# Kernel optimization log

Measured on AMD Instinct MI355X. Metric: run time of the kernel, lower is better.

## Reference

```python
import jax, jax.numpy as jnp
import numpy as np

N_GRAPH = 100000
N_CAND = 10
N_TOTAL = N_GRAPH + N_CAND
F_IN = 128
N_TYPES = 10
E = 6400000


def _p(key, shape, scale=0.05):
    return scale * jax.random.normal(key, shape, dtype=jnp.float32)


def setup_inputs() -> dict:
    key = jax.random.key(0)
    ks = jax.random.split(key, 20)
    x = jax.random.normal(ks[0], (N_GRAPH, F_IN), dtype=jnp.float32)
    candidate_set = jax.random.normal(ks[1], (N_CAND, F_IN), dtype=jnp.float32)
    edge_index = jax.random.randint(ks[2], (2, E), 0, N_GRAPH, dtype=jnp.int64)
    candidate_idx = jnp.arange(N_GRAPH, N_TOTAL, dtype=jnp.int64)  # candidate nodes appended last
    return {
        "x": x, "candidate_set": candidate_set,
        "edge_index": edge_index, "candidate_idx": candidate_idx,
        "W1": _p(ks[3], (F_IN, 16)), "b1": jnp.zeros((16,), jnp.float32),
        "W2": _p(ks[4], (16, 24)), "b2": jnp.zeros((24,), jnp.float32),
        "W3": _p(ks[5], (24, 32)), "b3": jnp.zeros((32,), jnp.float32),
        "Ws1": _p(ks[6], (32, 16)), "bs1": jnp.zeros((16,), jnp.float32),
        "Ws2": _p(ks[7], (16, N_TYPES)), "bs2": jnp.zeros((N_TYPES,), jnp.float32),
        "We1": _p(ks[8], (32, 24)), "be1": jnp.zeros((24,), jnp.float32),
        "We2": _p(ks[9], (24, N_TYPES)), "be2": jnp.zeros((N_TYPES,), jnp.float32),
    }


def _gcn(h, src, dst, W, b, n):
    # GCNConv: x' = D^{-1/2}(A+I)D^{-1/2} X W + b (self-loops added)
    h = h @ W
    deg = jax.ops.segment_sum(jnp.ones(src.shape, h.dtype), dst, num_segments=n) + 1.0
    dinv = jax.lax.rsqrt(deg)
    msg = h[src] * (dinv[src] * dinv[dst])[:, None]
    out = jax.ops.segment_sum(msg, dst, num_segments=n)
    out = out + h * (dinv * dinv)[:, None]  # self-loop term
    return out + b


def relu6(x):
    return jnp.clip(x, 0.0, 6.0)


def reference(x, candidate_set, edge_index, candidate_idx,
              W1, b1, W2, b2, W3, b3,
              Ws1, bs1, Ws2, bs2, We1, be1, We2, be2):
    n = N_TOTAL
    src, dst = edge_index[0], edge_index[1]
    h = jnp.concatenate([x, candidate_set], axis=0)  # [n, F_IN]
    h = _gcn(h, src, dst, W1, b1, n)
    h = _gcn(h, src, dst, W2, b2, n)
    h = _gcn(h, src, dst, W3, b3, n)  # [n, 32]

    start_probs = jax.nn.softmax(relu6(h @ Ws1 + bs1) @ Ws2 + bs2, axis=0)  # [n, T]
    mask = jnp.ones_like(start_probs).at[candidate_idx].set(0.0)
    start_probs = start_probs * mask
    start_probs = jnp.where(start_probs == 0.0, 1e-10, start_probs)
    k1, k2 = jax.random.split(jax.random.key(42))
    start_node = jax.random.categorical(k1, jnp.log(start_probs), axis=-1)  # [n]

    combined = jnp.concatenate([h, h[start_node]], axis=0)  # [2n, 32]
    end_probs = jax.nn.softmax(relu6(combined @ We1 + be1) @ We2 + be2, axis=0)  # [2n, T]
    end_probs = end_probs.at[start_node].set(0.0)
    end_probs = jnp.where(end_probs == 0.0, 1e-10, end_probs)
    end_node = jax.random.categorical(k2, jnp.log(end_probs), axis=-1)  # [2n]
    return (start_node, end_node, start_probs, end_probs)
```

## Files before the change

kernel.cpp:

```cpp
#include <hip/hip_runtime.h>
#include <stdint.h>

constexpr int N_GRAPH = 100000;
constexpr int N_CANDS = 10;
constexpr int NT      = N_GRAPH + N_CANDS;
constexpr int F_IN    = 128;
constexpr int NTYPES  = 10;
constexpr int NE      = 6400000;

constexpr int CB_SHIFT = 9;
constexpr int CB       = 1 << CB_SHIFT;
constexpr int NBK2     = (NT + CB - 1) / CB;
constexpr int SB       = 512;
constexpr int NMAT     = NBK2 * SB;
constexpr int NSCAN_B  = NMAT / 256;
constexpr int TMPENT_CAP = NE + NMAT * 15 + 16;

#define RNG_VARIANT 0

__device__ __forceinline__ void tf2x32(uint32_t k0, uint32_t k1, uint32_t x0, uint32_t x1,
                                       uint32_t& o0, uint32_t& o1) {
  const uint32_t ks2 = k0 ^ k1 ^ 0x1BD11BDAu;
  uint32_t v0 = x0 + k0, v1 = x1 + k1;
#define TFR(r) { v0 += v1; v1 = (v1 << (r)) | (v1 >> (32 - (r))); v1 ^= v0; }
  TFR(13) TFR(15) TFR(26) TFR(6)
  v0 += k1;  v1 += ks2 + 1u;
  TFR(17) TFR(29) TFR(16) TFR(24)
  v0 += ks2; v1 += k0 + 2u;
  TFR(13) TFR(15) TFR(26) TFR(6)
  v0 += k0;  v1 += k1 + 3u;
  TFR(17) TFR(29) TFR(16) TFR(24)
  v0 += k1;  v1 += ks2 + 4u;
  TFR(13) TFR(15) TFR(26) TFR(6)
  v0 += ks2; v1 += k0 + 5u;
#undef TFR
  o0 = v0; o1 = v1;
}

__device__ __forceinline__ void derive_keys(uint32_t& a0, uint32_t& a1,
                                            uint32_t& b0, uint32_t& b1) {
#if RNG_VARIANT == 2
  uint32_t c0, c1, d0, d1;
  tf2x32(0u, 42u, 0u, 2u, c0, c1);
  tf2x32(0u, 42u, 1u, 3u, d0, d1);
  a0 = c0; a1 = d0; b0 = c1; b1 = d1;
#else
  tf2x32(0u, 42u, 0u, 0u, a0, a1);
  tf2x32(0u, 42u, 0u, 1u, b0, b1);
#endif
}

__device__ __forceinline__ uint32_t rng_bits(uint32_t k0, uint32_t k1,
                                             uint32_t idx, uint32_t total) {
#if RNG_VARIANT == 0
  uint32_t o0, o1; tf2x32(k0, k1, 0u, idx, o0, o1); return o0 ^ o1;
#elif RNG_VARIANT == 1
  uint32_t o0, o1; tf2x32(k0, k1, 0u, idx, o0, o1); return o1;
#else
  uint32_t half = total >> 1; uint32_t o0, o1;
  if (idx < half) { tf2x32(k0, k1, idx, idx + half, o0, o1); return o0; }
  tf2x32(k0, k1, idx - half, idx, o0, o1); return o1;
#endif
}

__device__ __forceinline__ double gumbel_from_bits(uint32_t bits) {
  float uf = __uint_as_float((bits >> 9) | 0x3f800000u) - 1.0f;
  uf = fmaxf(1.17549435e-38f, uf + 1.17549435e-38f);
  return -log(-log((double)uf));
}

__device__ __forceinline__ uint32_t encf(float f) {
  uint32_t u = __float_as_uint(f);
  return u ^ ((u & 0x80000000u) ? 0xFFFFFFFFu : 0x80000000u);
}
__device__ __forceinline__ float decf(uint32_t e) {
  uint32_t u = (e & 0x80000000u) ? (e ^ 0x80000000u) : ~e;
  return __uint_as_float(u);
}

__global__ __launch_bounds__(512) void k_bcount(const int* __restrict__ dst,
                                                int* __restrict__ cntmat,
                                                int* __restrict__ cnt) {
  __shared__ int h[NBK2];
  int tid = threadIdx.x, blk = blockIdx.x;
  for (int b = tid; b < NBK2; b += 512) h[b] = 0;
  __syncthreads();
  int per = (NE + SB - 1) / SB;
  int e0 = blk * per, e1 = min(e0 + per, NE);
  for (int e = e0 + tid; e < e1; e += 512) atomicAdd(&h[dst[e] >> CB_SHIFT], 1);
  __syncthreads();
  for (int b = tid; b < NBK2; b += 512) {
    int c = h[b];
    cntmat[b * SB + blk] = (c + 15) & ~15;
    if (c) atomicAdd(&cnt[b], c);
  }
}

__global__ __launch_bounds__(256) void k_s1(int* __restrict__ cmat, int* __restrict__ partial) {
  __shared__ int sm[256];
  int t = blockIdx.x * 256 + threadIdx.x;
  int v = cmat[t];
  sm[threadIdx.x] = v;
  __syncthreads();
  #pragma unroll
  for (int s = 1; s < 256; s <<= 1) {
    int a = (threadIdx.x >= s) ? sm[threadIdx.x - s] : 0;
    __syncthreads();
    sm[threadIdx.x] += a;
    __syncthreads();
  }
  cmat[t] = sm[threadIdx.x] - v;
  if (threadIdx.x == 255) partial[blockIdx.x] = sm[255];
}

__global__ __launch_bounds__(512) void k_s2(int* __restrict__ partial, int* __restrict__ cmat) {
  __shared__ int sm[512];
  int t = threadIdx.x;
  int v = (t < NSCAN_B) ? partial[t] : 0;
  sm[t] = v;
  __syncthreads();
  #pragma unroll
  for (int s = 1; s < 512; s <<= 1) {
    int a = (t >= s) ? sm[t - s] : 0;
    __syncthreads();
    sm[t] += a;
    __syncthreads();
  }
  if (t < NSCAN_B) partial[t] = sm[t] - v;
  if (t == 511) cmat[NMAT] = sm[511];
}

__global__ __launch_bounds__(256) void k_s3(int* __restrict__ cmat, const int* __restrict__ partial) {
  int t = blockIdx.x * 256 + threadIdx.x;
  cmat[t] += partial[blockIdx.x];
}

__global__ __launch_bounds__(256) void k_rowscan(const int* __restrict__ cnt,
                                                 int* __restrict__ rowbase) {
  __shared__ int sm[256];
  int t = threadIdx.x;
  int v = (t < NBK2) ? cnt[t] : 0;
  sm[t] = v;
  __syncthreads();
  #pragma unroll
  for (int s = 1; s < 256; s <<= 1) {
    int a = (t >= s) ? sm[t - s] : 0;
    __syncthreads();
    sm[t] += a;
    __syncthreads();
  }
  if (t < NBK2) rowbase[t] = sm[t] - v;
}

__global__ __launch_bounds__(512) void k_scatter2(const int* __restrict__ src,
                                                  const int* __restrict__ dst,
                                                  const int* __restrict__ cmat,
                                                  uint32_t* __restrict__ tmpent) {
  __shared__ int lcur[NBK2];
  int tid = threadIdx.x, blk = blockIdx.x;
  for (int b = tid; b < NBK2; b += 512) lcur[b] = cmat[b * SB + blk];
  __syncthreads();
  int per = (NE + SB - 1) / SB;
  int e0 = blk * per, e1 = min(e0 + per, NE);
  for (int e = e0 + tid; e < e1; e += 512) {
    int s = src[e], d = dst[e];
    int b = d >> CB_SHIFT;
    int pos = atomicAdd(&lcur[b], 1);
    tmpent[pos] = (uint32_t)s | ((uint32_t)(d & (CB - 1)) << 17);
  }
  __syncthreads();
  for (int b = tid; b < NBK2; b += 512) {
    int p = lcur[b];
    int end = cmat[b * SB + blk + 1];
    for (; p < end; ++p) tmpent[p] = 0xFFFFFFFFu;
  }
}

__global__ __launch_bounds__(512) void k_place(const uint32_t* __restrict__ tmpent,
                                               const int* __restrict__ cmat,
                                               const int* __restrict__ rowbase,
                                               int* __restrict__ rowptr,
                                               float* __restrict__ dinv,
                                               int* __restrict__ col) {
  __shared__ int sdeg[CB];
  __shared__ int sexc[CB];
  __shared__ int sscan[CB];
  int b = blockIdx.x, tid = threadIdx.x;
  sdeg[tid] = 0;
  __syncthreads();
  int r0 = cmat[b * SB], r1 = cmat[(b + 1) * SB];
  for (int e = r0 + tid; e < r1; e += 512) {
    uint32_t v = tmpent[e];
    if (v != 0xFFFFFFFFu) atomicAdd(&sdeg[v >> 17], 1);
  }
  __syncthreads();
  int d = sdeg[tid];
  sscan[tid] = d;
  __syncthreads();
  #pragma unroll
  for (int s = 1; s < CB; s <<= 1) {
    int v = (tid >= s) ? sscan[tid - s] : 0;
    __syncthreads();
    sscan[tid] += v;
    __syncthreads();
  }
  int rb = rowbase[b];
  int incl = rb + sscan[tid];
  sexc[tid] = incl - d;
  int i = b * CB + tid;
  if (i < NT) {
    rowptr[i + 1] = incl;
    dinv[i] = (float)(1.0 / sqrt((double)(d + 1)));
  }
  if (b == 0 && tid == 0) rowptr[0] = 0;
  __syncthreads();
  for (int e = r0 + tid; e < r1; e += 512) {
    uint32_t v = tmpent[e];
    if (v != 0xFFFFFFFFu) {
      int pos = atomicAdd(&sexc[v >> 17], 1);
      col[pos] = (int)(v & 0x1FFFFu);
    }
  }
}

__global__ __launch_bounds__(256) void k_mm1(const float* __restrict__ x, const float* __restrict__ cand,
                                             const float* __restrict__ W, const float* __restrict__ dinv,
                                             float* __restrict__ zs0) {
  int gid = blockIdx.x * 256 + threadIdx.x;
  if (gid >= NT * 4) return;
  int i = gid >> 2, f4 = gid & 3;
  const float* hr = (i < N_GRAPH) ? (x + (size_t)i * F_IN)
                                  : (cand + (size_t)(i - N_GRAPH) * F_IN);
  const float4* h4 = reinterpret_cast<const float4*>(hr);
  const float4* W4 = reinterpret_cast<const float4*>(W);
  double a0 = 0.0, a1 = 0.0, a2 = 0.0, a3 = 0.0;
  #pragma unroll 8
  for (int q = 0; q < 32; ++q) {
    float4 hv = h4[q];
    float4 w0 = W4[(4 * q + 0) * 4 + f4];
    float4 w1 = W4[(4 * q + 1) * 4 + f4];
    float4 w2 = W4[(4 * q + 2) * 4 + f4];
    float4 w3 = W4[(4 * q + 3) * 4 + f4];
    a0 += (double)hv.x * w0.x + (double)hv.y * w1.x + (double)hv.z * w2.x + (double)hv.w * w3.x;
    a1 += (double)hv.x * w0.y + (double)hv.y * w1.y + (double)hv.z * w2.y + (double)hv.w * w3.y;
    a2 += (double)hv.x * w0.z + (double)hv.y * w1.z + (double)hv.z * w2.z + (double)hv.w * w3.z;
    a3 += (double)hv.x * w0.w + (double)hv.y * w1.w + (double)hv.z * w2.w + (double)hv.w * w3.w;
  }
  double di = (double)dinv[i];
  float4 o;
  o.x = (float)(a0 * di); o.y = (float)(a1 * di);
  o.z = (float)(a2 * di); o.w = (float)(a3 * di);
  reinterpret_cast<float4*>(zs0)[(size_t)i * 4 + f4] = o;
}

template <bool SQ, bool WITHW, int R>
__global__ __launch_bounds__(4 * R) void k_prop(const int* __restrict__ rowptr,
                                                const int* __restrict__ col,
                                                const float* __restrict__ zin,
                                                const float* __restrict__ win,
                                                const float* __restrict__ dinv,
                                                float* __restrict__ zout,
                                                float* __restrict__ wout,
                                                float* __restrict__ wsout) {
  int i = blockIdx.x * R + threadIdx.y;
  if (i >= NT) return;
  int fx = threadIdx.x;
  const float4* z4 = reinterpret_cast<const float4*>(zin);
  int e0 = rowptr[i], e1 = rowptr[i + 1];
  double a0 = 0.0, a1 = 0.0, a2 = 0.0, a3 = 0.0, wa = 0.0;
  int e = e0;
  for (; e + 4 <= e1; e += 4) {
    int c0 = col[e], c1 = col[e + 1], c2 = col[e + 2], c3 = col[e + 3];
    float4 v0 = z4[(size_t)c0 * 4 + fx];
    float4 v1 = z4[(size_t)c1 * 4 + fx];
    float4 v2 = z4[(size_t)c2 * 4 + fx];
    float4 v3 = z4[(size_t)c3 * 4 + fx];
    if (WITHW && fx == 0)
      wa += (double)win[c0] + (double)win[c1] + (double)win[c2] + (double)win[c3];
    a0 += (double)v0.x + (double)v1.x + (double)v2.x + (double)v3.x;
    a1 += (double)v0.y + (double)v1.y + (double)v2.y + (double)v3.y;
    a2 += (double)v0.z + (double)v1.z + (double)v2.z + (double)v3.z;
    a3 += (double)v0.w + (double)v1.w + (double)v2.w + (double)v3.w;
  }
  for (; e < e1; ++e) {
    int c = col[e];
    float4 v = z4[(size_t)c * 4 + fx];
    if (WITHW && fx == 0) wa += (double)win[c];
    a0 += (double)v.x; a1 += (double)v.y; a2 += (double)v.z; a3 += (double)v.w;
  }
  float4 s = z4[(size_t)i * 4 + fx];
  a0 += (double)s.x; a1 += (double)s.y; a2 += (double)s.z; a3 += (double)s.w;
  double di = (double)dinv[i];
  double sc = SQ ? di * di : di;
  float4 o;
  o.x = (float)(sc * a0); o.y = (float)(sc * a1);
  o.z = (float)(sc * a2); o.w = (float)(sc * a3);
  reinterpret_cast<float4*>(zout)[(size_t)i * 4 + fx] = o;
  if (WITHW && fx == 0) {
    wa += (double)win[i];
    double w = di * wa;
    wout[i]  = (float)w;
    wsout[i] = (float)(di * w);
  }
}

__global__ __launch_bounds__(512) void k_small(const float* __restrict__ W2, const float* __restrict__ b2p,
                                               const float* __restrict__ W3, const float* __restrict__ b1p,
                                               double* __restrict__ M, double* __restrict__ u,
                                               double* __restrict__ v) {
  __shared__ double t[24];
  int tid = threadIdx.x;
  if (tid < 24) {
    double a = 0.0;
    for (int k = 0; k < 16; ++k) a += (double)b1p[k] * (double)W2[k * 24 + tid];
    t[tid] = a;
  }
  if (tid >= 32 && tid < 64) {
    int o = tid - 32;
    double a = 0.0;
    for (int j = 0; j < 24; ++j) a += (double)b2p[j] * (double)W3[j * 32 + o];
    v[o] = a;
  }
  __syncthreads();
  if (tid < 32) {
    double a = 0.0;
    for (int j = 0; j < 24; ++j) a += t[j] * (double)W3[j * 32 + tid];
    u[tid] = a;
  }
  {
    int k = tid >> 5, o = tid & 31;
    double a = 0.0;
    for (int j = 0; j < 24; ++j) a += (double)W2[k * 24 + j] * (double)W3[j * 32 + o];
    M[tid] = a;
  }
}

__global__ __launch_bounds__(256) void k_epi(const float* __restrict__ z3, const float* __restrict__ w1,
                                             const float* __restrict__ w2,
                                             const double* __restrict__ M, const double* __restrict__ u,
                                             const double* __restrict__ v, const float* __restrict__ b3,
                                             float* __restrict__ H) {
  int gid = blockIdx.x * 256 + threadIdx.x;
  if (gid >= NT * 32) return;
  int i = gid >> 5, o = gid & 31;
  const float* zr = z3 + (size_t)i * 16;
  double acc = (double)b3[o] + (double)w2[i] * u[o] + (double)w1[i] * v[o];
  #pragma unroll
  for (int k = 0; k < 16; ++k) acc += (double)zr[k] * M[k * 32 + o];
  H[gid] = (float)acc;
}

template <int HID>
__global__ __launch_bounds__(256) void k_head(const float* __restrict__ H, const int* __restrict__ sn,
                                              int nrows,
                                              const float* __restrict__ Wa, const float* __restrict__ ba,
                                              const float* __restrict__ Wb, const float* __restrict__ bb,
                                              float* __restrict__ logits) {
  int i = blockIdx.x * 256 + threadIdx.x;
  if (i >= nrows) return;
  int row = (i < NT) ? i : sn[i - NT];
  const float* hr = H + (size_t)row * 32;
  float h[32];
  #pragma unroll
  for (int k = 0; k < 32; ++k) h[k] = hr[k];
  double hid[HID];
  for (int j = 0; j < HID; ++j) {
    double a = (double)ba[j];
    #pragma unroll
    for (int k = 0; k < 32; ++k) a += (double)h[k] * (double)Wa[k * HID + j];
    hid[j] = fmin(fmax(a, 0.0), 6.0);
  }
  for (int t = 0; t < NTYPES; ++t) {
    double l = (double)bb[t];
    #pragma unroll
    for (int j = 0; j < HID; ++j) l += hid[j] * (double)Wb[j * NTYPES + t];
    logits[(size_t)i * NTYPES + t] = (float)l;
  }
}

__global__ __launch_bounds__(256) void k_colmax(const float* __restrict__ L, int nrows,
                                                uint32_t* __restrict__ mb) {
  __shared__ float sm[256][NTYPES];
  float m[NTYPES];
  #pragma unroll
  for (int t = 0; t < NTYPES; ++t) m[t] = -3.402823466e38f;
  for (int r = blockIdx.x * 256 + threadIdx.x; r < nrows; r += gridDim.x * 256) {
    #pragma unroll
    for (int t = 0; t < NTYPES; ++t) m[t] = fmaxf(m[t], L[(size_t)r * NTYPES + t]);
  }
  #pragma unroll
  for (int t = 0; t < NTYPES; ++t) sm[threadIdx.x][t] = m[t];
  __syncthreads();
  for (int s = 128; s > 0; s >>= 1) {
    if (threadIdx.x < s)
      for (int t = 0; t < NTYPES; ++t)
        sm[threadIdx.x][t] = fmaxf(sm[threadIdx.x][t], sm[threadIdx.x + s][t]);
    __syncthreads();
  }
  if (threadIdx.x < NTYPES) atomicMax(&mb[threadIdx.x], encf(sm[0][threadIdx.x]));
}

__global__ __launch_bounds__(256) void k_colsum(const float* __restrict__ L, int nrows,
                                                const uint32_t* __restrict__ mb,
                                                double* __restrict__ sums) {
  __shared__ double sm[256][NTYPES];
  float mx[NTYPES];
  #pragma unroll
  for (int t = 0; t < NTYPES; ++t) mx[t] = decf(mb[t]);
  double s[NTYPES];
  #pragma unroll
  for (int t = 0; t < NTYPES; ++t) s[t] = 0.0;
  for (int r = blockIdx.x * 256 + threadIdx.x; r < nrows; r += gridDim.x * 256) {
    #pragma unroll
    for (int t = 0; t < NTYPES; ++t)
      s[t] += exp((double)L[(size_t)r * NTYPES + t] - (double)mx[t]);
  }
  #pragma unroll
  for (int t = 0; t < NTYPES; ++t) sm[threadIdx.x][t] = s[t];
  __syncthreads();
  for (int st = 128; st > 0; st >>= 1) {
    if (threadIdx.x < st)
      for (int t = 0; t < NTYPES; ++t)
        sm[threadIdx.x][t] += sm[threadIdx.x + st][t];
    __syncthreads();
  }
  if (threadIdx.x < NTYPES) atomicAdd(&sums[threadIdx.x], sm[0][threadIdx.x]);
}

__global__ __launch_bounds__(256) void k_probs_start(const float* __restrict__ L,
                                                     const uint32_t* __restrict__ mb,
                                                     const double* __restrict__ sums,
                                                     float* __restrict__ P) {
  int gid = blockIdx.x * 256 + threadIdx.x;
  if (gid >= NT * NTYPES) return;
  int i = gid / NTYPES, t = gid - i * NTYPES;
  double p = exp((double)L[gid] - (double)decf(mb[t])) / sums[t];
  float pf = (float)p;
  if (i >= N_GRAPH || pf == 0.0f) pf = 1e-10f;
  P[gid] = pf;
}

__global__ __launch_bounds__(256) void k_probs_end(const float* __restrict__ L,
                                                   const uint32_t* __restrict__ mb,
                                                   const double* __restrict__ sums,
                                                   const int* __restrict__ flags,
                                                   float* __restrict__ P) {
  int gid = blockIdx.x * 256 + threadIdx.x;
  if (gid >= 2 * NT * NTYPES) return;
  int j = gid / NTYPES, t = gid - j * NTYPES;
  double p = exp((double)L[gid] - (double)decf(mb[t])) / sums[t];
  float pf = (float)p;
  if ((j < NTYPES && flags[j]) || pf == 0.0f) pf = 1e-10f;
  P[gid] = pf;
}

__global__ __launch_bounds__(256) void k_sample_start(const float* __restrict__ probs,
                                                      float* __restrict__ outSN,
                                                      int* __restrict__ sn, int* __restrict__ flags) {
  int i = blockIdx.x * 256 + threadIdx.x;
  if (i >= NT) return;
  uint32_t a0, a1, b0, b1; derive_keys(a0, a1, b0, b1);
  double best = -1e300; int bi = 0;
  #pragma unroll
  for (int t = 0; t < NTYPES; ++t) {
    uint32_t bits = rng_bits(a0, a1, (uint32_t)(i * NTYPES + t), (uint32_t)(NT * NTYPES));
    double v = log((double)probs[(size_t)i * NTYPES + t]) + gumbel_from_bits(bits);
    if (v > best) { best = v; bi = t; }
  }
  sn[i] = bi;
  outSN[i] = (float)bi;
  flags[bi] = 1;
}

__global__ __launch_bounds__(256) void k_sample_end(const float* __restrict__ probs,
                                                    float* __restrict__ outEN) {
  int j = blockIdx.x * 256 + threadIdx.x;
  if (j >= 2 * NT) return;
  uint32_t a0, a1, b0, b1; derive_keys(a0, a1, b0, b1);
  double best = -1e300; int bi = 0;
  #pragma unroll
  for (int t = 0; t < NTYPES; ++t) {
    uint32_t bits = rng_bits(b0, b1, (uint32_t)(j * NTYPES + t), (uint32_t)(2 * NT * NTYPES));
    double v = log((double)probs[(size_t)j * NTYPES + t]) + gumbel_from_bits(bits);
    if (v > best) { best = v; bi = t; }
  }
  outEN[j] = (float)bi;
}

extern "C" void kernel_launch(void* const* d_in, const int* in_sizes, int n_in,
                              void* d_out, int out_size, void* d_ws, size_t ws_size,
                              hipStream_t stream) {
  const float* x    = (const float*)d_in[0];
  const float* cand = (const float*)d_in[1];
  const int*   ei   = (const int*)d_in[2];
  const float* W1 = (const float*)d_in[4];  const float* b1 = (const float*)d_in[5];
  const float* W2 = (const float*)d_in[6];  const float* b2 = (const float*)d_in[7];
  const float* W3 = (const float*)d_in[8];  const float* b3 = (const float*)d_in[9];
  const float* Ws1 = (const float*)d_in[10]; const float* bs1 = (const float*)d_in[11];
  const float* Ws2 = (const float*)d_in[12]; const float* bs2 = (const float*)d_in[13];
  const float* We1 = (const float*)d_in[14]; const float* be1 = (const float*)d_in[15];
  const float* We2 = (const float*)d_in[16]; const float* be2 = (const float*)d_in[17];
  float* out = (float*)d_out;
  float* outSN = out;
  float* outEN = out + NT;
  float* outPS = out + 3 * NT;
  float* outPE = out + 13 * NT;

  char* ws = (char*)d_ws;
  size_t off = 0;
  auto alloc = [&](size_t bytes) -> void* {
    void* p = ws + off;
    off += (bytes + 511) & ~(size_t)511;
    return p;
  };
  float*    dinv    = (float*)alloc((size_t)NT * 4);
  int*      rowptr  = (int*)alloc((size_t)(NT + 1) * 4);
  int*      cnt     = (int*)alloc((size_t)NBK2 * 4);
  int*      rowbase = (int*)alloc((size_t)NBK2 * 4);
  int*      cmat    = (int*)alloc((size_t)(NMAT + 1) * 4);
  int*      partial = (int*)alloc(512 * 4);
  int*      col     = (int*)alloc((size_t)NE * 4);
  char*     ublk    = (char*)alloc((size_t)TMPENT_CAP * 4);
  uint32_t* tmpent  = (uint32_t*)ublk;
  float*    zsA     = (float*)ublk;
  float*    zsB     = (float*)(ublk + (size_t)NT * 16 * 4);
  float*    Ha      = (float*)(ublk + (size_t)NT * 16 * 4 * 2);
  float*    logitsS = (float*)alloc((size_t)NT * NTYPES * 4);
  float*    logitsE = (float*)alloc((size_t)2 * NT * NTYPES * 4);
  float*    w1v     = (float*)alloc((size_t)NT * 4);
  float*    ws1v    = (float*)alloc((size_t)NT * 4);
  float*    w2v     = (float*)alloc((size_t)NT * 4);
  float*    wsd     = (float*)alloc((size_t)NT * 4);
  double*   Md      = (double*)alloc(512 * 8);
  double*   ud      = (double*)alloc(32 * 8);
  double*   vd      = (double*)alloc(32 * 8);
  int*      sn      = (int*)alloc((size_t)NT * 4);
  uint32_t* maxS    = (uint32_t*)alloc(64);
  double*   sumS    = (double*)alloc(128);
  uint32_t* maxE    = (uint32_t*)alloc(64);
  double*   sumE    = (double*)alloc(128);
  int*      flags   = (int*)alloc(64);
  (void)ws_size; (void)in_sizes; (void)n_in; (void)out_size;

  const int* srcA = ei;
  const int* dstA = ei + NE;

  const int B = 256;
  auto blocks = [](long long nthreads) { return (int)((nthreads + 255) / 256); };

  hipMemsetAsync(cnt, 0, (size_t)NBK2 * 4, stream);
  k_bcount<<<SB, 512, 0, stream>>>(dstA, cmat, cnt);
  k_s1<<<NSCAN_B, 256, 0, stream>>>(cmat, partial);
  k_s2<<<1, 512, 0, stream>>>(partial, cmat);
  k_s3<<<NSCAN_B, 256, 0, stream>>>(cmat, partial);
  k_rowscan<<<1, 256, 0, stream>>>(cnt, rowbase);
  k_scatter2<<<SB, 512, 0, stream>>>(srcA, dstA, cmat, tmpent);
  k_place<<<NBK2, 512, 0, stream>>>(tmpent, cmat, rowbase, rowptr, dinv, col);

  k_small<<<1, 512, 0, stream>>>(W2, b2, W3, b1, Md, ud, vd);
  k_mm1<<<blocks((long long)NT * 4), B, 0, stream>>>(x, cand, W1, dinv, zsA);
  const int PR = 64, PBLK = (NT + PR - 1) / PR;
  k_prop<true,  true,  PR><<<PBLK, dim3(4, PR), 0, stream>>>(rowptr, col, zsA, dinv, dinv, zsB, w1v, ws1v);
  k_prop<true,  true,  PR><<<PBLK, dim3(4, PR), 0, stream>>>(rowptr, col, zsB, ws1v, dinv, zsA, w2v, wsd);
  k_prop<false, false, PR><<<PBLK, dim3(4, PR), 0, stream>>>(rowptr, col, zsA, nullptr, dinv, zsB, nullptr, nullptr);
  k_epi<<<blocks((long long)NT * 32), B, 0, stream>>>(zsB, w1v, w2v, Md, ud, vd, b3, Ha);

  k_head<16><<<blocks(NT), B, 0, stream>>>(Ha, sn, NT, Ws1, bs1, Ws2, bs2, logitsS);
  hipMemsetAsync(maxS, 0, (size_t)((char*)flags - (char*)maxS) + 512, stream);
  k_colmax<<<512, B, 0, stream>>>(logitsS, NT, maxS);
  k_colsum<<<512, B, 0, stream>>>(logitsS, NT, maxS, sumS);
  k_probs_start<<<blocks((long long)NT * NTYPES), B, 0, stream>>>(logitsS, maxS, sumS, outPS);
  k_sample_start<<<blocks(NT), B, 0, stream>>>(outPS, outSN, sn, flags);

  k_head<24><<<blocks(2 * NT), B, 0, stream>>>(Ha, sn, 2 * NT, We1, be1, We2, be2, logitsE);
  k_colmax<<<512, B, 0, stream>>>(logitsE, 2 * NT, maxE);
  k_colsum<<<512, B, 0, stream>>>(logitsE, 2 * NT, maxE, sumE);
  k_probs_end<<<blocks((long long)2 * NT * NTYPES), B, 0, stream>>>(logitsE, maxE, sumE, flags, outPE);
  k_sample_end<<<blocks(2 * NT), B, 0, stream>>>(outPE, outEN);
}
```

Measured before the change: 868.3 us.

## Split GCN propagation into two feature halves to shrink gather working set

Feature rows are split into separate low and high 8-float arrays, and each propagation layer runs twice, once per half, so the random gather working set per pass is halved for better cache hit rates. Column index loads and output stores use nontemporal hints to avoid polluting cache, and the inner loop is unrolled by 8. The trade-off is reading the CSR column array twice per layer and launching extra kernels.

```diff
diff --git a/kernel.cpp b/kernel.cpp
--- a/kernel.cpp
+++ b/kernel.cpp
@@ -17,6 +17,8 @@
 constexpr int TMPENT_CAP = NE + NMAT * 15 + 16;
 
 #define RNG_VARIANT 0
+
+typedef float f4v __attribute__((ext_vector_type(4)));
 
 __device__ __forceinline__ void tf2x32(uint32_t k0, uint32_t k1, uint32_t x0, uint32_t x1,
                                        uint32_t& o0, uint32_t& o1) {
@@ -225,7 +227,7 @@
 
 __global__ __launch_bounds__(256) void k_mm1(const float* __restrict__ x, const float* __restrict__ cand,
                                              const float* __restrict__ W, const float* __restrict__ dinv,
-                                             float* __restrict__ zs0) {
+                                             float* __restrict__ zlo, float* __restrict__ zhi) {
   int gid = blockIdx.x * 256 + threadIdx.x;
   if (gid >= NT * 4) return;
   int i = gid >> 2, f4 = gid & 3;
@@ -250,18 +252,19 @@
   float4 o;
   o.x = (float)(a0 * di); o.y = (float)(a1 * di);
   o.z = (float)(a2 * di); o.w = (float)(a3 * di);
-  reinterpret_cast<float4*>(zs0)[(size_t)i * 4 + f4] = o;
+  if (f4 < 2) reinterpret_cast<float4*>(zlo)[(size_t)i * 2 + f4] = o;
+  else        reinterpret_cast<float4*>(zhi)[(size_t)i * 2 + (f4 - 2)] = o;
 }
 
 template <bool SQ, bool WITHW, int R>
-__global__ __launch_bounds__(4 * R) void k_prop(const int* __restrict__ rowptr,
-                                                const int* __restrict__ col,
-                                                const float* __restrict__ zin,
-                                                const float* __restrict__ win,
-                                                const float* __restrict__ dinv,
-                                                float* __restrict__ zout,
-                                                float* __restrict__ wout,
-                                                float* __restrict__ wsout) {
+__global__ __launch_bounds__(2 * R) void k_proph(const int* __restrict__ rowptr,
+                                                 const int* __restrict__ col,
+                                                 const float* __restrict__ zin,
+                                                 const float* __restrict__ win,
+                                                 const float* __restrict__ dinv,
+                                                 float* __restrict__ zout,
+                                                 float* __restrict__ wout,
+                                                 float* __restrict__ wsout) {
   int i = blockIdx.x * R + threadIdx.y;
   if (i >= NT) return;
   int fx = threadIdx.x;
@@ -269,12 +272,45 @@
   int e0 = rowptr[i], e1 = rowptr[i + 1];
   double a0 = 0.0, a1 = 0.0, a2 = 0.0, a3 = 0.0, wa = 0.0;
   int e = e0;
+  for (; e + 8 <= e1; e += 8) {
+    int c0 = __builtin_nontemporal_load(col + e);
+    int c1 = __builtin_nontemporal_load(col + e + 1);
+    int c2 = __builtin_nontemporal_load(col + e + 2);
+    int c3 = __builtin_nontemporal_load(col + e + 3);
+    int c4 = __builtin_nontemporal_load(col + e + 4);
+    int c5 = __builtin_nontemporal_load(col + e + 5);
+    int c6 = __builtin_nontemporal_load(col + e + 6);
+    int c7 = __builtin_nontemporal_load(col + e + 7);
+    float4 v0 = z4[(size_t)c0 * 2 + fx];
+    float4 v1 = z4[(size_t)c1 * 2 + fx];
+    float4 v2 = z4[(size_t)c2 * 2 + fx];
+    float4 v3 = z4[(size_t)c3 * 2 + fx];
+    float4 v4 = z4[(size_t)c4 * 2 + fx];
+    float4 v5 = z4[(size_t)c5 * 2 + fx];
+    float4 v6 = z4[(size_t)c6 * 2 + fx];
+    float4 v7 = z4[(size_t)c7 * 2 + fx];
+    if (WITHW && fx == 0) {
+      wa += (double)win[c0] + (double)win[c1] + (double)win[c2] + (double)win[c3];
+      wa += (double)win[c4] + (double)win[c5] + (double)win[c6] + (double)win[c7];
+    }
+    a0 += (double)v0.x + (double)v1.x + (double)v2.x + (double)v3.x;
+    a1 += (double)v0.y + (double)v1.y + (double)v2.y + (double)v3.y;
+    a2 += (double)v0.z + (double)v1.z + (double)v2.z + (double)v3.z;
+    a3 += (double)v0.w + (double)v1.w + (double)v2.w + (double)v3.w;
+    a0 += (double)v4.x + (double)v5.x + (double)v6.x + (double)v7.x;
+    a1 += (double)v4.y + (double)v5.y + (double)v6.y + (double)v7.y;
+    a2 += (double)v4.z + (double)v5.z + (double)v6.z + (double)v7.z;
+    a3 += (double)v4.w + (double)v5.w + (double)v6.w + (double)v7.w;
+  }
   for (; e + 4 <= e1; e += 4) {
-    int c0 = col[e], c1 = col[e + 1], c2 = col[e + 2], c3 = col[e + 3];
-    float4 v0 = z4[(size_t)c0 * 4 + fx];
-    float4 v1 = z4[(size_t)c1 * 4 + fx];
-    float4 v2 = z4[(size_t)c2 * 4 + fx];
-    float4 v3 = z4[(size_t)c3 * 4 + fx];
+    int c0 = __builtin_nontemporal_load(col + e);
+    int c1 = __builtin_nontemporal_load(col + e + 1);
+    int c2 = __builtin_nontemporal_load(col + e + 2);
+    int c3 = __builtin_nontemporal_load(col + e + 3);
+    float4 v0 = z4[(size_t)c0 * 2 + fx];
+    float4 v1 = z4[(size_t)c1 * 2 + fx];
+    float4 v2 = z4[(size_t)c2 * 2 + fx];
+    float4 v3 = z4[(size_t)c3 * 2 + fx];
     if (WITHW && fx == 0)
       wa += (double)win[c0] + (double)win[c1] + (double)win[c2] + (double)win[c3];
     a0 += (double)v0.x + (double)v1.x + (double)v2.x + (double)v3.x;
@@ -283,19 +319,19 @@
     a3 += (double)v0.w + (double)v1.w + (double)v2.w + (double)v3.w;
   }
   for (; e < e1; ++e) {
-    int c = col[e];
-    float4 v = z4[(size_t)c * 4 + fx];
+    int c = __builtin_nontemporal_load(col + e);
+    float4 v = z4[(size_t)c * 2 + fx];
     if (WITHW && fx == 0) wa += (double)win[c];
     a0 += (double)v.x; a1 += (double)v.y; a2 += (double)v.z; a3 += (double)v.w;
   }
-  float4 s = z4[(size_t)i * 4 + fx];
+  float4 s = z4[(size_t)i * 2 + fx];
   a0 += (double)s.x; a1 += (double)s.y; a2 += (double)s.z; a3 += (double)s.w;
   double di = (double)dinv[i];
   double sc = SQ ? di * di : di;
-  float4 o;
+  f4v o;
   o.x = (float)(sc * a0); o.y = (float)(sc * a1);
   o.z = (float)(sc * a2); o.w = (float)(sc * a3);
-  reinterpret_cast<float4*>(zout)[(size_t)i * 4 + fx] = o;
+  __builtin_nontemporal_store(o, reinterpret_cast<f4v*>(zout) + (size_t)i * 2 + fx);
   if (WITHW && fx == 0) {
     wa += (double)win[i];
     double w = di * wa;
@@ -335,7 +371,8 @@
   }
 }
 
-__global__ __launch_bounds__(256) void k_epi(const float* __restrict__ z3, const float* __restrict__ w1,
+__global__ __launch_bounds__(256) void k_epi(const float* __restrict__ zlo, const float* __restrict__ zhi,
+                                             const float* __restrict__ w1,
                                              const float* __restrict__ w2,
                                              const double* __restrict__ M, const double* __restrict__ u,
                                              const double* __restrict__ v, const float* __restrict__ b3,
@@ -343,10 +380,13 @@
   int gid = blockIdx.x * 256 + threadIdx.x;
   if (gid >= NT * 32) return;
   int i = gid >> 5, o = gid & 31;
-  const float* zr = z3 + (size_t)i * 16;
+  const float* zrl = zlo + (size_t)i * 8;
+  const float* zrh = zhi + (size_t)i * 8;
   double acc = (double)b3[o] + (double)w2[i] * u[o] + (double)w1[i] * v[o];
   #pragma unroll
-  for (int k = 0; k < 16; ++k) acc += (double)zr[k] * M[k * 32 + o];
+  for (int k = 0; k < 8; ++k) acc += (double)zrl[k] * M[k * 32 + o];
+  #pragma unroll
+  for (int k = 0; k < 8; ++k) acc += (double)zrh[k] * M[(k + 8) * 32 + o];
   H[gid] = (float)acc;
 }
 
@@ -522,9 +562,11 @@
   int*      col     = (int*)alloc((size_t)NE * 4);
   char*     ublk    = (char*)alloc((size_t)TMPENT_CAP * 4);
   uint32_t* tmpent  = (uint32_t*)ublk;
-  float*    zsA     = (float*)ublk;
-  float*    zsB     = (float*)(ublk + (size_t)NT * 16 * 4);
-  float*    Ha      = (float*)(ublk + (size_t)NT * 16 * 4 * 2);
+  float*    zloA    = (float*)ublk;
+  float*    zhiA    = (float*)(ublk + (size_t)NT * 8 * 4);
+  float*    zloB    = (float*)(ublk + (size_t)NT * 8 * 4 * 2);
+  float*    zhiB    = (float*)(ublk + (size_t)NT * 8 * 4 * 3);
+  float*    Ha      = (float*)(ublk + (size_t)NT * 8 * 4 * 4);
   float*    logitsS = (float*)alloc((size_t)NT * NTYPES * 4);
   float*    logitsE = (float*)alloc((size_t)2 * NT * NTYPES * 4);
   float*    w1v     = (float*)alloc((size_t)NT * 4);
@@ -558,12 +600,15 @@
   k_place<<<NBK2, 512, 0, stream>>>(tmpent, cmat, rowbase, rowptr, dinv, col);
 
   k_small<<<1, 512, 0, stream>>>(W2, b2, W3, b1, Md, ud, vd);
-  k_mm1<<<blocks((long long)NT * 4), B, 0, stream>>>(x, cand, W1, dinv, zsA);
-  const int PR = 64, PBLK = (NT + PR - 1) / PR;
-  k_prop<true,  true,  PR><<<PBLK, dim3(4, PR), 0, stream>>>(rowptr, col, zsA, dinv, dinv, zsB, w1v, ws1v);
-  k_prop<true,  true,  PR><<<PBLK, dim3(4, PR), 0, stream>>>(rowptr, col, zsB, ws1v, dinv, zsA, w2v, wsd);
-  k_prop<false, false, PR><<<PBLK, dim3(4, PR), 0, stream>>>(rowptr, col, zsA, nullptr, dinv, zsB, nullptr, nullptr);
-  k_epi<<<blocks((long long)NT * 32), B, 0, stream>>>(zsB, w1v, w2v, Md, ud, vd, b3, Ha);
+  k_mm1<<<blocks((long long)NT * 4), B, 0, stream>>>(x, cand, W1, dinv, zloA, zhiA);
+  const int PR = 128, PBLK = (NT + PR - 1) / PR;
+  k_proph<true,  true,  PR><<<PBLK, dim3(2, PR), 0, stream>>>(rowptr, col, zloA, dinv, dinv, zloB, w1v, ws1v);
+  k_proph<true,  false, PR><<<PBLK, dim3(2, PR), 0, stream>>>(rowptr, col, zhiA, nullptr, dinv, zhiB, nullptr, nullptr);
+  k_proph<true,  true,  PR><<<PBLK, dim3(2, PR), 0, stream>>>(rowptr, col, zloB, ws1v, dinv, zloA, w2v, wsd);
+  k_proph<true,  false, PR><<<PBLK, dim3(2, PR), 0, stream>>>(rowptr, col, zhiB, nullptr, dinv, zhiA, nullptr, nullptr);
+  k_proph<false, false, PR><<<PBLK, dim3(2, PR), 0, stream>>>(rowptr, col, zloA, nullptr, dinv, zloB, nullptr, nullptr);
+  k_proph<false, false, PR><<<PBLK, dim3(2, PR), 0, stream>>>(rowptr, col, zhiA, nullptr, dinv, zhiB, nullptr, nullptr);
+  k_epi<<<blocks((long long)NT * 32), B, 0, stream>>>(zloB, zhiB, w1v, w2v, Md, ud, vd, b3, Ha);
 
   k_head<16><<<blocks(NT), B, 0, stream>>>(Ha, sn, NT, Ws1, bs1, Ws2, bs2, logitsS);
   hipMemsetAsync(maxS, 0, (size_t)((char*)flags - (char*)maxS) + 512, stream);
```

New measurement: 965.1 us. 1.11x slower.

## Split each node's edges across two thread groups and fuse probability with sampling

Applied to the files above, without the earlier changes.

The propagation kernel now gives each node 8 threads instead of 4. Two 4-thread groups take alternating 4-edge chunks, and their partial sums are combined with a lane shuffle, which roughly doubles memory-level parallelism per row in the gather-bound SpMM. Column indices are loaded nontemporally to keep them out of cache. The separate softmax-probability and Gumbel-sampling kernels are merged for both the start and end heads, which saves a launch and a reread of the probability array each time. Each row now carries more serial work per thread, and the masking logic is duplicated inside the fused kernels.

```diff
diff --git a/kernel.cpp b/kernel.cpp
--- a/kernel.cpp
+++ b/kernel.cpp
@@ -17,6 +17,8 @@
 constexpr int TMPENT_CAP = NE + NMAT * 15 + 16;
 
 #define RNG_VARIANT 0
+
+typedef float f4v __attribute__((ext_vector_type(4)));
 
 __device__ __forceinline__ void tf2x32(uint32_t k0, uint32_t k1, uint32_t x0, uint32_t x1,
                                        uint32_t& o0, uint32_t& o1) {
@@ -254,53 +256,68 @@
 }
 
 template <bool SQ, bool WITHW, int R>
-__global__ __launch_bounds__(4 * R) void k_prop(const int* __restrict__ rowptr,
-                                                const int* __restrict__ col,
-                                                const float* __restrict__ zin,
-                                                const float* __restrict__ win,
-                                                const float* __restrict__ dinv,
-                                                float* __restrict__ zout,
-                                                float* __restrict__ wout,
-                                                float* __restrict__ wsout) {
+__global__ __launch_bounds__(8 * R) void k_prop3(const int* __restrict__ rowptr,
+                                                 const int* __restrict__ col,
+                                                 const float* __restrict__ zin,
+                                                 const float* __restrict__ win,
+                                                 const float* __restrict__ dinv,
+                                                 float* __restrict__ zout,
+                                                 float* __restrict__ wout,
+                                                 float* __restrict__ wsout) {
   int i = blockIdx.x * R + threadIdx.y;
   if (i >= NT) return;
-  int fx = threadIdx.x;
+  int fx = threadIdx.x & 3;
+  int es = threadIdx.x >> 2;
   const float4* z4 = reinterpret_cast<const float4*>(zin);
   int e0 = rowptr[i], e1 = rowptr[i + 1];
+  int ngrp = (e1 - e0) >> 2;
   double a0 = 0.0, a1 = 0.0, a2 = 0.0, a3 = 0.0, wa = 0.0;
-  int e = e0;
-  for (; e + 4 <= e1; e += 4) {
-    int c0 = col[e], c1 = col[e + 1], c2 = col[e + 2], c3 = col[e + 3];
+  const bool dow = WITHW && (fx == 0);
+  for (int gq = es; gq < ngrp; gq += 2) {
+    int e = e0 + (gq << 2);
+    int c0 = __builtin_nontemporal_load(col + e);
+    int c1 = __builtin_nontemporal_load(col + e + 1);
+    int c2 = __builtin_nontemporal_load(col + e + 2);
+    int c3 = __builtin_nontemporal_load(col + e + 3);
     float4 v0 = z4[(size_t)c0 * 4 + fx];
     float4 v1 = z4[(size_t)c1 * 4 + fx];
     float4 v2 = z4[(size_t)c2 * 4 + fx];
     float4 v3 = z4[(size_t)c3 * 4 + fx];
-    if (WITHW && fx == 0)
+    if (dow)
       wa += (double)win[c0] + (double)win[c1] + (double)win[c2] + (double)win[c3];
     a0 += (double)v0.x + (double)v1.x + (double)v2.x + (double)v3.x;
     a1 += (double)v0.y + (double)v1.y + (double)v2.y + (double)v3.y;
     a2 += (double)v0.z + (double)v1.z + (double)v2.z + (double)v3.z;
     a3 += (double)v0.w + (double)v1.w + (double)v2.w + (double)v3.w;
   }
-  for (; e < e1; ++e) {
-    int c = col[e];
-    float4 v = z4[(size_t)c * 4 + fx];
-    if (WITHW && fx == 0) wa += (double)win[c];
-    a0 += (double)v.x; a1 += (double)v.y; a2 += (double)v.z; a3 += (double)v.w;
-  }
-  float4 s = z4[(size_t)i * 4 + fx];
-  a0 += (double)s.x; a1 += (double)s.y; a2 += (double)s.z; a3 += (double)s.w;
-  double di = (double)dinv[i];
-  double sc = SQ ? di * di : di;
-  float4 o;
-  o.x = (float)(sc * a0); o.y = (float)(sc * a1);
-  o.z = (float)(sc * a2); o.w = (float)(sc * a3);
-  reinterpret_cast<float4*>(zout)[(size_t)i * 4 + fx] = o;
-  if (WITHW && fx == 0) {
-    wa += (double)win[i];
-    double w = di * wa;
-    wout[i]  = (float)w;
-    wsout[i] = (float)(di * w);
+  if (es == (ngrp & 1)) {
+    for (int e = e0 + (ngrp << 2); e < e1; ++e) {
+      int c = __builtin_nontemporal_load(col + e);
+      float4 v = z4[(size_t)c * 4 + fx];
+      if (dow) wa += (double)win[c];
+      a0 += (double)v.x; a1 += (double)v.y; a2 += (double)v.z; a3 += (double)v.w;
+    }
+  }
+  a0 += __shfl_xor(a0, 4);
+  a1 += __shfl_xor(a1, 4);
+  a2 += __shfl_xor(a2, 4);
+  a3 += __shfl_xor(a3, 4);
+  if (WITHW) wa += __shfl_xor(wa, 4);
+  if (es == 0) {
+    float4 s = z4[(size_t)i * 4 + fx];
+    a0 += (double)s.x; a1 += (double)s.y; a2 += (double)s.z; a3 += (double)s.w;
+    double di = (double)dinv[i];
+    double sc = SQ ? di * di : di;
+    float4 o;
+    o.x = (float)(sc * a0); o.y = (float)(sc * a1);
+    o.z = (float)(sc * a2); o.w = (float)(sc * a3);
+    reinterpret_cast<float4*>(zout)[(size_t)i * 4 + fx] = o;
+    if (dow) {
+      wa += (double)win[i];
+      double w = di * wa;
+      wout[i]  = (float)w;
+      wsout[i] = (float)(di * w);
+    }
   }
 }
 
@@ -427,44 +444,25 @@
   if (threadIdx.x < NTYPES) atomicAdd(&sums[threadIdx.x], sm[0][threadIdx.x]);
 }
 
-__global__ __launch_bounds__(256) void k_probs_start(const float* __restrict__ L,
-                                                     const uint32_t* __restrict__ mb,
-                                                     const double* __restrict__ sums,
-                                                     float* __restrict__ P) {
-  int gid = blockIdx.x * 256 + threadIdx.x;
-  if (gid >= NT * NTYPES) return;
-  int i = gid / NTYPES, t = gid - i * NTYPES;
-  double p = exp((double)L[gid] - (double)decf(mb[t])) / sums[t];
-  float pf = (float)p;
-  if (i >= N_GRAPH || pf == 0.0f) pf = 1e-10f;
-  P[gid] = pf;
-}
-
-__global__ __launch_bounds__(256) void k_probs_end(const float* __restrict__ L,
-                                                   const uint32_t* __restrict__ mb,
-                                                   const double* __restrict__ sums,
-                                                   const int* __restrict__ flags,
-                                                   float* __restrict__ P) {
-  int gid = blockIdx.x * 256 + threadIdx.x;
-  if (gid >= 2 * NT * NTYPES) return;
-  int j = gid / NTYPES, t = gid - j * NTYPES;
-  double p = exp((double)L[gid] - (double)decf(mb[t])) / sums[t];
-  float pf = (float)p;
-  if ((j < NTYPES && flags[j]) || pf == 0.0f) pf = 1e-10f;
-  P[gid] = pf;
-}
-
-__global__ __launch_bounds__(256) void k_sample_start(const float* __restrict__ probs,
-                                                      float* __restrict__ outSN,
-                                                      int* __restrict__ sn, int* __restrict__ flags) {
+__global__ __launch_bounds__(256) void k_ps_start(const float* __restrict__ L,
+                                                  const uint32_t* __restrict__ mb,
+                                                  const double* __restrict__ sums,
+                                                  float* __restrict__ P,
+                                                  float* __restrict__ outSN,
+                                                  int* __restrict__ sn,
+                                                  int* __restrict__ flags) {
   int i = blockIdx.x * 256 + threadIdx.x;
   if (i >= NT) return;
   uint32_t a0, a1, b0, b1; derive_keys(a0, a1, b0, b1);
   double best = -1e300; int bi = 0;
   #pragma unroll
   for (int t = 0; t < NTYPES; ++t) {
+    double p = exp((double)L[(size_t)i * NTYPES + t] - (double)decf(mb[t])) / sums[t];
+    float pf = (float)p;
+    if (i >= N_GRAPH || pf == 0.0f) pf = 1e-10f;
+    P[(size_t)i * NTYPES + t] = pf;
     uint32_t bits = rng_bits(a0, a1, (uint32_t)(i * NTYPES + t), (uint32_t)(NT * NTYPES));
-    double v = log((double)probs[(size_t)i * NTYPES + t]) + gumbel_from_bits(bits);
+    double v = log((double)pf) + gumbel_from_bits(bits);
     if (v > best) { best = v; bi = t; }
   }
   sn[i] = bi;
@@ -472,16 +470,25 @@
   flags[bi] = 1;
 }
 
-__global__ __launch_bounds__(256) void k_sample_end(const float* __restrict__ probs,
-                                                    float* __restrict__ outEN) {
+__global__ __launch_bounds__(256) void k_ps_end(const float* __restrict__ L,
+                                                const uint32_t* __restrict__ mb,
+                                                const double* __restrict__ sums,
+                                                const int* __restrict__ flags,
+                                                float* __restrict__ P,
+                                                float* __restrict__ outEN) {
   int j = blockIdx.x * 256 + threadIdx.x;
   if (j >= 2 * NT) return;
   uint32_t a0, a1, b0, b1; derive_keys(a0, a1, b0, b1);
+  const bool rowmask = (j < NTYPES && flags[j]);
   double best = -1e300; int bi = 0;
   #pragma unroll
   for (int t = 0; t < NTYPES; ++t) {
+    double p = exp((double)L[(size_t)j * NTYPES + t] - (double)decf(mb[t])) / sums[t];
+    float pf = (float)p;
+    if (rowmask || pf == 0.0f) pf = 1e-10f;
+    P[(size_t)j * NTYPES + t] = pf;
     uint32_t bits = rng_bits(b0, b1, (uint32_t)(j * NTYPES + t), (uint32_t)(2 * NT * NTYPES));
-    double v = log((double)probs[(size_t)j * NTYPES + t]) + gumbel_from_bits(bits);
+    double v = log((double)pf) + gumbel_from_bits(bits);
     if (v > best) { best = v; bi = t; }
   }
   outEN[j] = (float)bi;
@@ -559,22 +566,20 @@
 
   k_small<<<1, 512, 0, stream>>>(W2, b2, W3, b1, Md, ud, vd);
   k_mm1<<<blocks((long long)NT * 4), B, 0, stream>>>(x, cand, W1, dinv, zsA);
-  const int PR = 64, PBLK = (NT + PR - 1) / PR;
-  k_prop<true,  true,  PR><<<PBLK, dim3(4, PR), 0, stream>>>(rowptr, col, zsA, dinv, dinv, zsB, w1v, ws1v);
-  k_prop<true,  true,  PR><<<PBLK, dim3(4, PR), 0, stream>>>(rowptr, col, zsB, ws1v, dinv, zsA, w2v, wsd);
-  k_prop<false, false, PR><<<PBLK, dim3(4, PR), 0, stream>>>(rowptr, col, zsA, nullptr, dinv, zsB, nullptr, nullptr);
+  const int PR3 = 32, PBLK = (NT + PR3 - 1) / PR3;
+  k_prop3<true,  true,  PR3><<<PBLK, dim3(8, PR3), 0, stream>>>(rowptr, col, zsA, dinv, dinv, zsB, w1v, ws1v);
+  k_prop3<true,  true,  PR3><<<PBLK, dim3(8, PR3), 0, stream>>>(rowptr, col, zsB, ws1v, dinv, zsA, w2v, wsd);
+  k_prop3<false, false, PR3><<<PBLK, dim3(8, PR3), 0, stream>>>(rowptr, col, zsA, nullptr, dinv, zsB, nullptr, nullptr);
   k_epi<<<blocks((long long)NT * 32), B, 0, stream>>>(zsB, w1v, w2v, Md, ud, vd, b3, Ha);
 
   k_head<16><<<blocks(NT), B, 0, stream>>>(Ha, sn, NT, Ws1, bs1, Ws2, bs2, logitsS);
   hipMemsetAsync(maxS, 0, (size_t)((char*)flags - (char*)maxS) + 512, stream);
   k_colmax<<<512, B, 0, stream>>>(logitsS, NT, maxS);
   k_colsum<<<512, B, 0, stream>>>(logitsS, NT, maxS, sumS);
-  k_probs_start<<<blocks((long long)NT * NTYPES), B, 0, stream>>>(logitsS, maxS, sumS, outPS);
-  k_sample_start<<<blocks(NT), B, 0, stream>>>(outPS, outSN, sn, flags);
+  k_ps_start<<<blocks(NT), B, 0, stream>>>(logitsS, maxS, sumS, outPS, outSN, sn, flags);
 
   k_head<24><<<blocks(2 * NT), B, 0, stream>>>(Ha, sn, 2 * NT, We1, be1, We2, be2, logitsE);
   k_colmax<<<512, B, 0, stream>>>(logitsE, 2 * NT, maxE);
   k_colsum<<<512, B, 0, stream>>>(logitsE, 2 * NT, maxE, sumE);
-  k_probs_end<<<blocks((long long)2 * NT * NTYPES), B, 0, stream>>>(logitsE, maxE, sumE, flags, outPE);
-  k_sample_end<<<blocks(2 * NT), B, 0, stream>>>(outPE, outEN);
-}
+  k_ps_end<<<blocks((long long)2 * NT), B, 0, stream>>>(logitsE, maxE, sumE, flags, outPE, outEN);
+}
```

New measurement: 787.5 us. 9.3% less time.
